# Kernel tuning notes

Hardware: AMD Instinct MI355X
Metric: run time of the kernel (lower is better)

## Reference

```python
import jax, jax.numpy as jnp
import numpy as np

GRID_SIZE = 8
SPLINE_ORDER = 3
LAYERS = [256, 512, 512, 256]  # [input_dim] + hidden_dims
BATCH = 8192
BN_EPS = 1e-5


def make_grid(in_features):
    # efficient-kan/torchkan grid: uniform on [-1, 1] extended by spline_order on each side
    h = 2.0 / GRID_SIZE
    g = jnp.arange(-SPLINE_ORDER, GRID_SIZE + SPLINE_ORDER + 1, dtype=jnp.float32) * h - 1.0
    return jnp.broadcast_to(g, (in_features, g.shape[0]))  # (In, G + 2k + 1)


def b_splines(x, grid):
    # x: (B, In), grid: (In, G + 2k + 1) -> bases: (B, In, G + k)
    xg = x[:, :, None]
    bases = ((xg >= grid[:, :-1]) & (xg < grid[:, 1:])).astype(x.dtype)
    for k in range(1, SPLINE_ORDER + 1):
        left = (xg - grid[:, : -(k + 1)]) / (grid[:, k:-1] - grid[:, : -(k + 1)])
        right = (grid[:, k + 1 :] - xg) / (grid[:, k + 1 :] - grid[:, 1:-k])
        bases = left * bases[:, :, :-1] + right * bases[:, :, 1:]
    return bases


def kan_linear(x, grid, base_w, spline_w):
    # base path: GELU (exact, matching torch.nn.GELU) then linear
    base_out = jax.nn.gelu(x, approximate=False) @ base_w.T
    spline_out = jnp.einsum('bik,oik->bo', b_splines(x, grid), spline_w)
    return base_out + spline_out


def setup_inputs() -> dict:
    key = jax.random.key(0)
    ks = jax.random.split(key, 16)
    inp = {'x': jax.random.normal(ks[0], (BATCH, LAYERS[0]), dtype=jnp.float32)}
    n_bases = GRID_SIZE + SPLINE_ORDER
    for i, (fin, fout) in enumerate(zip(LAYERS[:-1], LAYERS[1:])):
        scale = 1.0 / np.sqrt(fin)
        inp[f'grid{i}'] = make_grid(fin)
        inp[f'base_w{i}'] = jax.random.normal(ks[1 + 3 * i], (fout, fin), dtype=jnp.float32) * scale
        inp[f'spline_w{i}'] = jax.random.normal(ks[2 + 3 * i], (fout, fin, n_bases), dtype=jnp.float32) * (0.1 * scale)
    d_out = LAYERS[-1]
    inp['bn_gamma'] = jnp.ones((d_out,), dtype=jnp.float32)
    inp['bn_beta'] = jnp.zeros((d_out,), dtype=jnp.float32)
    inp['bn_mean'] = jax.random.normal(ks[10], (d_out,), dtype=jnp.float32) * 0.1
    inp['bn_var'] = jax.random.uniform(ks[11], (d_out,), dtype=jnp.float32, minval=0.5, maxval=1.5)
    return inp


def reference(x, grid0, base_w0, spline_w0, grid1, base_w1, spline_w1, grid2, base_w2, spline_w2, bn_gamma, bn_beta, bn_mean, bn_var):
    h = kan_linear(x, grid0, base_w0, spline_w0)
    h = kan_linear(h, grid1, base_w1, spline_w1)
    h = kan_linear(h, grid2, base_w2, spline_w2)
    # BatchNorm1d in eval mode (running stats); Dropout is identity at inference
    return bn_gamma * (h - bn_mean) * jax.lax.rsqrt(bn_var + BN_EPS) + bn_beta
```

## Files before the change

kernel.cpp:

```cpp
#include <hip/hip_runtime.h>
#include <hip/hip_bf16.h>
#include <cstdint>


typedef unsigned short ushort_t;
typedef __bf16 bf16x8 __attribute__((ext_vector_type(8)));
typedef float f32x4 __attribute__((ext_vector_type(4)));

__device__ __forceinline__ ushort_t f2bf(float f) {
    __bf16 h = (__bf16)f;
    return __builtin_bit_cast(ushort_t, h);
}

__device__ __forceinline__ void gload_lds16(const void* g, void* lds) {
    __builtin_amdgcn_global_load_lds(
        (const __attribute__((address_space(1))) unsigned int*)(uintptr_t)g,
        (__attribute__((address_space(3))) unsigned int*)(unsigned int)(uintptr_t)lds,
        16, 0, 0);
}

__device__ __forceinline__ void expand12(float x, ushort_t* o) {
    float x3 = x * x * x;
    float y  = 0.7978845608028654f * (x + 0.044715f * x3);
    float e  = __expf(2.0f * y);
    float th = 1.0f - 2.0f / (e + 1.0f);
    o[0] = f2bf(0.5f * x * (1.0f + th));
    float xs = (x + 1.75f) * 4.0f;
#pragma unroll
    for (int j = 0; j < 11; ++j) {
        float t  = xs - (float)j;
        float a  = fabsf(t - 2.0f);
        float p1 = (3.0f * a - 6.0f) * a * a + 4.0f;
        float c  = 2.0f - a;
        float p2 = c * c * c;
        float v  = (a <= 1.0f) ? p1 : fmaxf(p2, 0.0f);
        o[1 + j] = f2bf(v * (1.0f / 6.0f));
    }
}

template <bool SUM>
__global__ __launch_bounds__(256) void expand_kernel(
    const float* __restrict__ X0, const float* __restrict__ X1,
    ushort_t* __restrict__ A, int total2)
{
    int idx = blockIdx.x * 256 + threadIdx.x;
    if (idx >= total2) return;
    float2 h = *(const float2*)(X0 + 2 * (size_t)idx);
    if (SUM) {
        float2 h2 = *(const float2*)(X1 + 2 * (size_t)idx);
        h.x += h2.x; h.y += h2.y;
    }
    union { ushort_t us[24]; uint4 v[3]; } pk;
    expand12(h.x, pk.us);
    expand12(h.y, pk.us + 12);
    uint4* dst = (uint4*)(A + (size_t)idx * 24);
    dst[0] = pk.v[0]; dst[1] = pk.v[1]; dst[2] = pk.v[2];
}

__global__ __launch_bounds__(256) void pack_w_kernel(
    const float* __restrict__ bw, const float* __restrict__ sw,
    ushort_t* __restrict__ W, int total)
{
    int idx = blockIdx.x * 256 + threadIdx.x;
    if (idx >= total) return;
    union { ushort_t us[12]; uint2 v[3]; } pk;
    pk.us[0] = f2bf(bw[idx]);
    const float* s = sw + (size_t)idx * 11;
#pragma unroll
    for (int k = 0; k < 11; ++k) pk.us[1 + k] = f2bf(s[k]);
    uint2* dst = (uint2*)(W + (size_t)idx * 12);
    dst[0] = pk.v[0]; dst[1] = pk.v[1]; dst[2] = pk.v[2];
}

__global__ __launch_bounds__(256, 2) void gemm_kernel(
    const ushort_t* __restrict__ A,
    const ushort_t* __restrict__ W,
    float* __restrict__ C,
    int M, int N, int K, int kcps)
{
    __shared__ __align__(16) ushort_t As[128 * 64];
    __shared__ __align__(16) ushort_t Bs[128 * 64];

    const int t   = threadIdx.x;
    const int l   = t & 63;
    const int w   = t >> 6;
    const int wm  = w >> 1;
    const int wn  = w & 1;
    const int l15 = l & 15;
    const int q   = l >> 4;
    const int blockM = blockIdx.x * 128;
    const int blockN = blockIdx.y * 128;
    const int kb0 = blockIdx.z * kcps, kb1 = kb0 + kcps;
    float* Cz = C + (size_t)blockIdx.z * M * N;

    f32x4 acc[4][4];
#pragma unroll
    for (int i = 0; i < 4; ++i)
#pragma unroll
        for (int j = 0; j < 4; ++j) acc[i][j] = (f32x4){0.f, 0.f, 0.f, 0.f};

    for (int kb = kb0; kb < kb1; ++kb) {
        const int k0 = kb << 6;
#pragma unroll
        for (int it = 0; it < 4; ++it) {
            int s   = it * 256 + t;
            int row = s >> 3, c = s & 7;
            int g   = c ^ (row & 7);
            gload_lds16(A + ((size_t)(blockM + row) * K + k0 + g * 8), &As[s * 8]);
        }
#pragma unroll
        for (int it = 0; it < 4; ++it) {
            int s   = it * 256 + t;
            int row = s >> 3, c = s & 7;
            int g   = c ^ (row & 7);
            gload_lds16(W + ((size_t)(blockN + row) * K + k0 + g * 8), &Bs[s * 8]);
        }
        __syncthreads();

#pragma unroll
        for (int ks = 0; ks < 2; ++ks) {
            const int kc = ks * 4 + q;
            bf16x8 af[4], bf[4];
#pragma unroll
            for (int mi = 0; mi < 4; ++mi) {
                int m  = wm * 64 + mi * 16 + l15;
                int cs = kc ^ (m & 7);
                af[mi] = *(const bf16x8*)&As[(size_t)(m * 8 + cs) * 8];
            }
#pragma unroll
            for (int ni = 0; ni < 4; ++ni) {
                int n  = wn * 64 + ni * 16 + l15;
                int cs = kc ^ (n & 7);
                bf[ni] = *(const bf16x8*)&Bs[(size_t)(n * 8 + cs) * 8];
            }
#pragma unroll
            for (int mi = 0; mi < 4; ++mi)
#pragma unroll
                for (int ni = 0; ni < 4; ++ni)
                    acc[mi][ni] = __builtin_amdgcn_mfma_f32_16x16x32_bf16(
                        af[mi], bf[ni], acc[mi][ni], 0, 0, 0);
        }
        __syncthreads();
    }

#pragma unroll
    for (int ni = 0; ni < 4; ++ni) {
        int n = blockN + wn * 64 + ni * 16 + l15;
#pragma unroll
        for (int mi = 0; mi < 4; ++mi) {
            int mb = blockM + wm * 64 + mi * 16 + q * 4;
#pragma unroll
            for (int r = 0; r < 4; ++r)
                Cz[(size_t)(mb + r) * N + n] = acc[mi][ni][r];
        }
    }
}

__global__ __launch_bounds__(256) void bn_reduce_kernel(
    const float4* __restrict__ Q0, const float4* __restrict__ Q1,
    const float4* __restrict__ Q2, const float4* __restrict__ Q3,
    const float* __restrict__ gamma, const float* __restrict__ beta,
    const float* __restrict__ mean,  const float* __restrict__ var,
    float4* __restrict__ out, int n4)
{
    int i = blockIdx.x * 256 + threadIdx.x;
    if (i >= n4) return;
    float4 a = Q0[i], b = Q1[i], c = Q2[i], d = Q3[i];
    int nb = (i * 4) & 255;
    float4 g  = *(const float4*)(gamma + nb);
    float4 be = *(const float4*)(beta + nb);
    float4 mn = *(const float4*)(mean + nb);
    float4 vr = *(const float4*)(var + nb);
    float4 o;
    o.x = g.x * rsqrtf(vr.x + 1e-5f) * (a.x + b.x + c.x + d.x - mn.x) + be.x;
    o.y = g.y * rsqrtf(vr.y + 1e-5f) * (a.y + b.y + c.y + d.y - mn.y) + be.y;
    o.z = g.z * rsqrtf(vr.z + 1e-5f) * (a.z + b.z + c.z + d.z - mn.z) + be.z;
    o.w = g.w * rsqrtf(vr.w + 1e-5f) * (a.w + b.w + c.w + d.w - mn.w) + be.w;
    out[i] = o;
}

extern "C" void kernel_launch(void* const* d_in, const int* in_sizes, int n_in,
                              void* d_out, int out_size, void* d_ws, size_t ws_size,
                              hipStream_t stream) {
    const float* x     = (const float*)d_in[0];
    const float* bw0   = (const float*)d_in[2];
    const float* sw0   = (const float*)d_in[3];
    const float* bw1   = (const float*)d_in[5];
    const float* sw1   = (const float*)d_in[6];
    const float* bw2   = (const float*)d_in[8];
    const float* sw2   = (const float*)d_in[9];
    const float* gamma = (const float*)d_in[10];
    const float* beta  = (const float*)d_in[11];
    const float* mean  = (const float*)d_in[12];
    const float* var   = (const float*)d_in[13];

    char* ws = (char*)d_ws;
    ushort_t* Abuf = (ushort_t*)(ws);
    ushort_t* W0   = (ushort_t*)(ws + 100663296);
    ushort_t* W1   = (ushort_t*)(ws + 103809024);
    ushort_t* W2   = (ushort_t*)(ws + 110100480);
    float*    P0   = (float*)(ws + 113246208);
    float*    P1   = (float*)(ws + 130023424);
    float*    Q0   = (float*)(ws + 113246208);
    float*    Q1   = (float*)(ws + 121634816);
    float*    Q2   = (float*)(ws + 130023424);
    float*    Q3   = (float*)(ws + 138412032);
    float*    out  = (float*)d_out;

    pack_w_kernel<<<(512 * 256 + 255) / 256, 256, 0, stream>>>(bw0, sw0, W0, 512 * 256);
    pack_w_kernel<<<(512 * 512 + 255) / 256, 256, 0, stream>>>(bw1, sw1, W1, 512 * 512);
    pack_w_kernel<<<(256 * 512 + 255) / 256, 256, 0, stream>>>(bw2, sw2, W2, 256 * 512);

    expand_kernel<false><<<4096, 256, 0, stream>>>(x, nullptr, Abuf, 8192 * 256 / 2);
    {
        dim3 g(64, 4, 2);
        gemm_kernel<<<g, 256, 0, stream>>>(Abuf, W0, P0, 8192, 512, 3072, 24);
    }
    expand_kernel<true><<<8192, 256, 0, stream>>>(P0, P1, Abuf, 8192 * 512 / 2);
    {
        dim3 g(64, 4, 2);
        gemm_kernel<<<g, 256, 0, stream>>>(Abuf, W1, P0, 8192, 512, 6144, 48);
    }
    expand_kernel<true><<<8192, 256, 0, stream>>>(P0, P1, Abuf, 8192 * 512 / 2);
    {
        dim3 g(64, 2, 4);
        gemm_kernel<<<g, 256, 0, stream>>>(Abuf, W2, Q0, 8192, 256, 6144, 24);
    }
    bn_reduce_kernel<<<2048, 256, 0, stream>>>(
        (const float4*)Q0, (const float4*)Q1, (const float4*)Q2, (const float4*)Q3,
        gamma, beta, mean, var, (float4*)out, 8192 * 256 / 4);
}
```

Baseline: 303.1 us.

## Fuse spline basis expansion into GEMM prologue and merge weight packing

Measured after the change: 621.9 us. 105% more time.

```diff
diff --git a/kernel.cpp b/kernel.cpp
--- a/kernel.cpp
+++ b/kernel.cpp
@@ -10,13 +10,6 @@
 __device__ __forceinline__ ushort_t f2bf(float f) {
     __bf16 h = (__bf16)f;
     return __builtin_bit_cast(ushort_t, h);
-}
-
-__device__ __forceinline__ void gload_lds16(const void* g, void* lds) {
-    __builtin_amdgcn_global_load_lds(
-        (const __attribute__((address_space(1))) unsigned int*)(uintptr_t)g,
-        (__attribute__((address_space(3))) unsigned int*)(unsigned int)(uintptr_t)lds,
-        16, 0, 0);
 }
 
 __device__ __forceinline__ void expand12(float x, ushort_t* o) {
@@ -38,60 +31,54 @@
     }
 }
 
-template <bool SUM>
-__global__ __launch_bounds__(256) void expand_kernel(
-    const float* __restrict__ X0, const float* __restrict__ X1,
-    ushort_t* __restrict__ A, int total2)
+__device__ __forceinline__ void expand_pair(float hx, float hy, uint4* ev) {
+    union { ushort_t us[24]; uint4 v[3]; } pk;
+    expand12(hx, pk.us);
+    expand12(hy, pk.us + 12);
+    ev[0] = pk.v[0]; ev[1] = pk.v[1]; ev[2] = pk.v[2];
+}
+
+__global__ __launch_bounds__(256) void pack_all_kernel(
+    const float* __restrict__ bw0, const float* __restrict__ sw0, ushort_t* __restrict__ W0,
+    const float* __restrict__ bw1, const float* __restrict__ sw1, ushort_t* __restrict__ W1,
+    const float* __restrict__ bw2, const float* __restrict__ sw2, ushort_t* __restrict__ W2)
 {
     int idx = blockIdx.x * 256 + threadIdx.x;
-    if (idx >= total2) return;
-    float2 h = *(const float2*)(X0 + 2 * (size_t)idx);
-    if (SUM) {
-        float2 h2 = *(const float2*)(X1 + 2 * (size_t)idx);
-        h.x += h2.x; h.y += h2.y;
-    }
-    union { ushort_t us[24]; uint4 v[3]; } pk;
-    expand12(h.x, pk.us);
-    expand12(h.y, pk.us + 12);
-    uint4* dst = (uint4*)(A + (size_t)idx * 24);
+    const float* bw; const float* sw; ushort_t* W; int local;
+    if (idx < 131072)      { bw = bw0; sw = sw0; W = W0; local = idx; }
+    else if (idx < 393216) { bw = bw1; sw = sw1; W = W1; local = idx - 131072; }
+    else                   { bw = bw2; sw = sw2; W = W2; local = idx - 393216; }
+    union { ushort_t us[12]; uint2 v[3]; } pk;
+    pk.us[0] = f2bf(bw[local]);
+    const float* s = sw + (size_t)local * 11;
+#pragma unroll
+    for (int k = 0; k < 11; ++k) pk.us[1 + k] = f2bf(s[k]);
+    uint2* dst = (uint2*)(W + (size_t)local * 12);
     dst[0] = pk.v[0]; dst[1] = pk.v[1]; dst[2] = pk.v[2];
 }
 
-__global__ __launch_bounds__(256) void pack_w_kernel(
-    const float* __restrict__ bw, const float* __restrict__ sw,
-    ushort_t* __restrict__ W, int total)
+template <bool SUM>
+__global__ __launch_bounds__(256, 2) void kan_gemm_kernel(
+    const float* __restrict__ X0, const ushort_t* __restrict__ Wm,
+    float* __restrict__ C, int M, int fin, int N, int spl, size_t xoff)
 {
-    int idx = blockIdx.x * 256 + threadIdx.x;
-    if (idx >= total) return;
-    union { ushort_t us[12]; uint2 v[3]; } pk;
-    pk.us[0] = f2bf(bw[idx]);
-    const float* s = sw + (size_t)idx * 11;
-#pragma unroll
-    for (int k = 0; k < 11; ++k) pk.us[1 + k] = f2bf(s[k]);
-    uint2* dst = (uint2*)(W + (size_t)idx * 12);
-    dst[0] = pk.v[0]; dst[1] = pk.v[1]; dst[2] = pk.v[2];
-}
-
-__global__ __launch_bounds__(256, 2) void gemm_kernel(
-    const ushort_t* __restrict__ A,
-    const ushort_t* __restrict__ W,
-    float* __restrict__ C,
-    int M, int N, int K, int kcps)
-{
-    __shared__ __align__(16) ushort_t As[128 * 64];
-    __shared__ __align__(16) ushort_t Bs[128 * 64];
+    __shared__ __align__(16) ushort_t As[128 * 24 * 8];
+    __shared__ __align__(16) ushort_t Bs[128 * 8 * 8];
 
     const int t   = threadIdx.x;
     const int l   = t & 63;
     const int w   = t >> 6;
-    const int wm  = w >> 1;
+    const int wmm = w >> 1;
     const int wn  = w & 1;
     const int l15 = l & 15;
     const int q   = l >> 4;
+    const int K   = fin * 12;
     const int blockM = blockIdx.x * 128;
     const int blockN = blockIdx.y * 128;
-    const int kb0 = blockIdx.z * kcps, kb1 = kb0 + kcps;
-    float* Cz = C + (size_t)blockIdx.z * M * N;
+    const int z   = blockIdx.z;
+    const int slab0 = z * spl;
+    const int xr  = t >> 3;
+    const int fp  = t & 7;
 
     f32x4 acc[4][4];
 #pragma unroll
@@ -99,56 +86,138 @@
 #pragma unroll
         for (int j = 0; j < 4; ++j) acc[i][j] = (f32x4){0.f, 0.f, 0.f, 0.f};
 
-    for (int kb = kb0; kb < kb1; ++kb) {
-        const int k0 = kb << 6;
-#pragma unroll
-        for (int it = 0; it < 4; ++it) {
-            int s   = it * 256 + t;
-            int row = s >> 3, c = s & 7;
-            int g   = c ^ (row & 7);
-            gload_lds16(A + ((size_t)(blockM + row) * K + k0 + g * 8), &As[s * 8]);
-        }
-#pragma unroll
-        for (int it = 0; it < 4; ++it) {
-            int s   = it * 256 + t;
-            int row = s >> 3, c = s & 7;
-            int g   = c ^ (row & 7);
-            gload_lds16(W + ((size_t)(blockN + row) * K + k0 + g * 8), &Bs[s * 8]);
-        }
-        __syncthreads();
-
-#pragma unroll
-        for (int ks = 0; ks < 2; ++ks) {
-            const int kc = ks * 4 + q;
-            bf16x8 af[4], bf[4];
-#pragma unroll
-            for (int mi = 0; mi < 4; ++mi) {
-                int m  = wm * 64 + mi * 16 + l15;
-                int cs = kc ^ (m & 7);
-                af[mi] = *(const bf16x8*)&As[(size_t)(m * 8 + cs) * 8];
+    const ushort_t* wp[4];
+#pragma unroll
+    for (int it = 0; it < 4; ++it) {
+        int row = it * 32 + xr;
+        int g   = fp ^ (row & 7);
+        wp[it] = Wm + (size_t)(blockN + row) * K + g * 8;
+    }
+    const float* xp[4];
+#pragma unroll
+    for (int i = 0; i < 4; ++i)
+        xp[i] = X0 + (size_t)(blockM + i * 32 + xr) * fin + fp * 2;
+
+    uint4  breg[4];
+    float2 xa[4];
+    uint4  ereg[4][3];
+
+#pragma unroll
+    for (int it = 0; it < 4; ++it)
+        breg[it] = *(const uint4*)(wp[it] + (size_t)(slab0 * 3) * 64);
+#pragma unroll
+    for (int i = 0; i < 4; ++i) {
+        xa[i] = *(const float2*)(xp[i] + (size_t)slab0 * 16);
+        if (SUM) {
+            float2 b = *(const float2*)(xp[i] + xoff + (size_t)slab0 * 16);
+            xa[i].x += b.x; xa[i].y += b.y;
+        }
+    }
+#pragma unroll
+    for (int i = 0; i < 4; ++i) expand_pair(xa[i].x, xa[i].y, ereg[i]);
+    {
+        int ns = (spl > 1) ? (slab0 + 1) : slab0;
+#pragma unroll
+        for (int i = 0; i < 4; ++i) {
+            xa[i] = *(const float2*)(xp[i] + (size_t)ns * 16);
+            if (SUM) {
+                float2 b = *(const float2*)(xp[i] + xoff + (size_t)ns * 16);
+                xa[i].x += b.x; xa[i].y += b.y;
             }
-#pragma unroll
-            for (int ni = 0; ni < 4; ++ni) {
-                int n  = wn * 64 + ni * 16 + l15;
-                int cs = kc ^ (n & 7);
-                bf[ni] = *(const bf16x8*)&Bs[(size_t)(n * 8 + cs) * 8];
+        }
+    }
+
+#define MFMA_BLOCK(KB)                                                         \
+    {                                                                          \
+        _Pragma("unroll")                                                      \
+        for (int ks = 0; ks < 2; ++ks) {                                       \
+            const int kc  = (KB) * 8 + ks * 4 + q;                             \
+            const int kc8 = ks * 4 + q;                                        \
+            bf16x8 af[4], bfr[4];                                              \
+            _Pragma("unroll")                                                  \
+            for (int mi = 0; mi < 4; ++mi) {                                   \
+                int m  = wmm * 64 + mi * 16 + l15;                             \
+                int cs = kc ^ (m & 7);                                         \
+                af[mi] = *(const bf16x8*)&As[(size_t)(m * 24 + cs) * 8];       \
+            }                                                                  \
+            _Pragma("unroll")                                                  \
+            for (int ni = 0; ni < 4; ++ni) {                                   \
+                int n  = wn * 64 + ni * 16 + l15;                              \
+                int cs = kc8 ^ (n & 7);                                        \
+                bfr[ni] = *(const bf16x8*)&Bs[(size_t)(n * 8 + cs) * 8];       \
+            }                                                                  \
+            _Pragma("unroll")                                                  \
+            for (int mi = 0; mi < 4; ++mi)                                     \
+                _Pragma("unroll")                                              \
+                for (int ni = 0; ni < 4; ++ni)                                 \
+                    acc[mi][ni] = __builtin_amdgcn_mfma_f32_16x16x32_bf16(     \
+                        af[mi], bfr[ni], acc[mi][ni], 0, 0, 0);                \
+        }                                                                      \
+    }
+
+    for (int sl = 0; sl < spl; ++sl) {
+        const int kbg = (slab0 + sl) * 3;
+        __syncthreads();
+#pragma unroll
+        for (int i = 0; i < 4; ++i) {
+            int m = i * 32 + xr;
+#pragma unroll
+            for (int j = 0; j < 3; ++j) {
+                int cs = (fp * 3 + j) ^ (m & 7);
+                *(uint4*)&As[(size_t)(m * 24 + cs) * 8] = ereg[i][j];
             }
-#pragma unroll
-            for (int mi = 0; mi < 4; ++mi)
-#pragma unroll
-                for (int ni = 0; ni < 4; ++ni)
-                    acc[mi][ni] = __builtin_amdgcn_mfma_f32_16x16x32_bf16(
-                        af[mi], bf[ni], acc[mi][ni], 0, 0, 0);
-        }
-        __syncthreads();
-    }
-
+        }
+#pragma unroll
+        for (int it = 0; it < 4; ++it) ((uint4*)Bs)[it * 256 + t] = breg[it];
+        __syncthreads();
+
+#pragma unroll
+        for (int it = 0; it < 4; ++it)
+            breg[it] = *(const uint4*)(wp[it] + (size_t)(kbg + 1) * 64);
+        MFMA_BLOCK(0)
+
+        if (sl + 1 < spl) {
+#pragma unroll
+            for (int i = 0; i < 4; ++i) expand_pair(xa[i].x, xa[i].y, ereg[i]);
+            int ns = (sl + 2 < spl) ? (slab0 + sl + 2) : (slab0 + spl - 1);
+#pragma unroll
+            for (int i = 0; i < 4; ++i) {
+                xa[i] = *(const float2*)(xp[i] + (size_t)ns * 16);
+                if (SUM) {
+                    float2 b = *(const float2*)(xp[i] + xoff + (size_t)ns * 16);
+                    xa[i].x += b.x; xa[i].y += b.y;
+                }
+            }
+        }
+        __syncthreads();
+#pragma unroll
+        for (int it = 0; it < 4; ++it) ((uint4*)Bs)[it * 256 + t] = breg[it];
+        __syncthreads();
+#pragma unroll
+        for (int it = 0; it < 4; ++it)
+            breg[it] = *(const uint4*)(wp[it] + (size_t)(kbg + 2) * 64);
+        MFMA_BLOCK(1)
+        __syncthreads();
+#pragma unroll
+        for (int it = 0; it < 4; ++it) ((uint4*)Bs)[it * 256 + t] = breg[it];
+        __syncthreads();
+        {
+            int nkb = (sl + 1 < spl) ? (kbg + 3) : (kbg + 2);
+#pragma unroll
+            for (int it = 0; it < 4; ++it)
+                breg[it] = *(const uint4*)(wp[it] + (size_t)nkb * 64);
+        }
+        MFMA_BLOCK(2)
+    }
+#undef MFMA_BLOCK
+
+    float* Cz = C + (size_t)z * M * N;
 #pragma unroll
     for (int ni = 0; ni < 4; ++ni) {
         int n = blockN + wn * 64 + ni * 16 + l15;
 #pragma unroll
         for (int mi = 0; mi < 4; ++mi) {
-            int mb = blockM + wm * 64 + mi * 16 + q * 4;
+            int mb = blockM + wmm * 64 + mi * 16 + q * 4;
 #pragma unroll
             for (int r = 0; r < 4; ++r)
                 Cz[(size_t)(mb + r) * N + n] = acc[mi][ni][r];
@@ -195,38 +264,33 @@
     const float* var   = (const float*)d_in[13];
 
     char* ws = (char*)d_ws;
-    ushort_t* Abuf = (ushort_t*)(ws);
-    ushort_t* W0   = (ushort_t*)(ws + 100663296);
-    ushort_t* W1   = (ushort_t*)(ws + 103809024);
-    ushort_t* W2   = (ushort_t*)(ws + 110100480);
-    float*    P0   = (float*)(ws + 113246208);
-    float*    P1   = (float*)(ws + 130023424);
-    float*    Q0   = (float*)(ws + 113246208);
-    float*    Q1   = (float*)(ws + 121634816);
-    float*    Q2   = (float*)(ws + 130023424);
-    float*    Q3   = (float*)(ws + 138412032);
-    float*    out  = (float*)d_out;
-
-    pack_w_kernel<<<(512 * 256 + 255) / 256, 256, 0, stream>>>(bw0, sw0, W0, 512 * 256);
-    pack_w_kernel<<<(512 * 512 + 255) / 256, 256, 0, stream>>>(bw1, sw1, W1, 512 * 512);
-    pack_w_kernel<<<(256 * 512 + 255) / 256, 256, 0, stream>>>(bw2, sw2, W2, 256 * 512);
-
-    expand_kernel<false><<<4096, 256, 0, stream>>>(x, nullptr, Abuf, 8192 * 256 / 2);
+    ushort_t* W0 = (ushort_t*)(ws);
+    ushort_t* W1 = (ushort_t*)(ws + 3145728);
+    ushort_t* W2 = (ushort_t*)(ws + 9437184);
+    float*    P  = (float*)(ws + 12582912);
+    float*    R  = (float*)(ws + 46137344);
+    float*    Q  = (float*)(ws + 79691776);
+    float*    out = (float*)d_out;
+
+    const size_t MN = (size_t)8192 * 512;
+    const size_t QN = (size_t)8192 * 256;
+
+    pack_all_kernel<<<2048, 256, 0, stream>>>(bw0, sw0, W0, bw1, sw1, W1, bw2, sw2, W2);
+
     {
         dim3 g(64, 4, 2);
-        gemm_kernel<<<g, 256, 0, stream>>>(Abuf, W0, P0, 8192, 512, 3072, 24);
-    }
-    expand_kernel<true><<<8192, 256, 0, stream>>>(P0, P1, Abuf, 8192 * 512 / 2);
+        kan_gemm_kernel<false><<<g, 256, 0, stream>>>(x, W0, P, 8192, 256, 512, 8, 0);
+    }
     {
         dim3 g(64, 4, 2);
-        gemm_kernel<<<g, 256, 0, stream>>>(Abuf, W1, P0, 8192, 512, 6144, 48);
-    }
-    expand_kernel<true><<<8192, 256, 0, stream>>>(P0, P1, Abuf, 8192 * 512 / 2);
+        kan_gemm_kernel<true><<<g, 256, 0, stream>>>(P, W1, R, 8192, 512, 512, 16, MN);
+    }
     {
         dim3 g(64, 2, 4);
-        gemm_kernel<<<g, 256, 0, stream>>>(Abuf, W2, Q0, 8192, 256, 6144, 24);
+        kan_gemm_kernel<true><<<g, 256, 0, stream>>>(R, W2, Q, 8192, 512, 256, 8, MN);
     }
     bn_reduce_kernel<<<2048, 256, 0, stream>>>(
-        (const float4*)Q0, (const float4*)Q1, (const float4*)Q2, (const float4*)Q3,
-        gamma, beta, mean, var, (float4*)out, 8192 * 256 / 4);
-}
+        (const float4*)Q, (const float4*)(Q + QN), (const float4*)(Q + 2 * QN),
+        (const float4*)(Q + 3 * QN), gamma, beta, mean, var,
+        (float4*)out, 8192 * 256 / 4);
+}
```
